# Performance work log

Measured on AMD Instinct MI355X. Metric: run time of the kernel, lower is better.

Reference implementation:

```python
import jax, jax.numpy as jnp
import numpy as np

N_NODES = 100000
N_EDGES = 1600000
N_GRAPHS = 2048
D = 128
H = 128
EPS = 1e-5


def gcn_conv(x, src, dst, W, b, n):
    # x: [N, Din], W: [Din, Dout]; GCN with added self-loops and symmetric norm
    xw = x @ W                                       # [N, Dout]
    deg = jnp.zeros((n,), x.dtype).at[dst].add(1.0) + 1.0  # deg of A+I (counted on dst)
    dinv = jax.lax.rsqrt(deg)                        # [N]
    norm = dinv[src] * dinv[dst]                     # [E]
    msg = xw[src] * norm[:, None]                    # [E, Dout] gather + scale
    agg = jax.ops.segment_sum(msg, dst, num_segments=n)
    agg = agg + xw * (dinv * dinv)[:, None]          # self-loop contribution
    return agg + b


def gru_step_h0(x, W_ih, W_hh, b_ih, b_hh):
    # single GRU step with h0 = 0 (PyTorch gate order r, z, n)
    h0 = jnp.zeros_like(x)
    gi = x @ W_ih.T + b_ih                           # [G, 3H]
    gh = h0 @ W_hh.T + b_hh                          # [G, 3H] (zeros + b_hh)
    ir, iz, inn = jnp.split(gi, 3, axis=-1)
    hr, hz, hn = jnp.split(gh, 3, axis=-1)
    r = jax.nn.sigmoid(ir + hr)
    z = jax.nn.sigmoid(iz + hz)
    n = jnp.tanh(inn + r * hn)
    return (1.0 - z) * n + z * h0


def setup_inputs() -> dict:
    key = jax.random.key(0)
    ks = jax.random.split(key, 10)
    x = jax.random.normal(ks[0], (N_NODES, D), jnp.float32)
    edge_index = jax.random.randint(ks[1], (2, N_EDGES), 0, N_NODES, jnp.int32)
    batch = jnp.sort(jax.random.randint(ks[2], (N_NODES,), 0, N_GRAPHS, jnp.int32))
    s = 1.0 / np.sqrt(H)
    return {
        "x": x,
        "edge_index": edge_index,
        "batch": batch,
        "W1": jax.random.normal(ks[3], (D, H), jnp.float32) * s,
        "b1": jnp.zeros((H,), jnp.float32),
        "W2": jax.random.normal(ks[4], (H, H), jnp.float32) * s,
        "b2": jnp.zeros((H,), jnp.float32),
        "W_ih": jax.random.normal(ks[5], (3 * H, H), jnp.float32) * s,
        "W_hh": jax.random.normal(ks[6], (3 * H, H), jnp.float32) * s,
        "b_ih": jnp.zeros((3 * H,), jnp.float32),
        "b_hh": jnp.zeros((3 * H,), jnp.float32),
        "W_lin": jax.random.normal(ks[7], (1, H), jnp.float32) * s,
        "b_lin": jnp.zeros((1,), jnp.float32),
    }


def reference(x, edge_index, batch, W1, b1, W2, b2, W_ih, W_hh, b_ih, b_hh, W_lin, b_lin):
    src, dst = edge_index[0], edge_index[1]
    n = x.shape[0]
    h = jax.nn.relu(gcn_conv(x, src, dst, W1, b1, n))
    h = gcn_conv(h, src, dst, W2, b2, n)
    # global_mean_pool over graph ids
    sums = jax.ops.segment_sum(h, batch, num_segments=N_GRAPHS)
    cnts = jax.ops.segment_sum(jnp.ones((n,), h.dtype), batch, num_segments=N_GRAPHS)
    g = sums / jnp.maximum(cnts, 1.0)[:, None]       # [G, H]
    # dropout p=0.5 in eval mode -> identity
    g = gru_step_h0(g, W_ih, W_hh, b_ih, b_hh)
    g = jax.nn.relu(g)
    mu = jnp.mean(g, axis=-1, keepdims=True)
    var = jnp.mean(jnp.square(g - mu), axis=-1, keepdims=True)
    g = (g - mu) * jax.lax.rsqrt(var + EPS)          # layer_norm, no affine
    return g @ W_lin.T + b_lin                       # [G, 1]
```

## Files before the change

### kernel.cpp

```cpp
#include <hip/hip_runtime.h>
#include <hip/hip_bf16.h>
#include <math.h>

#define DHID 128
#define SH 8
#define BIN_T 8192
#define CAPSH 13

typedef __attribute__((ext_vector_type(8))) short bf16x8;
typedef __attribute__((ext_vector_type(4))) float f32x4;

__device__ __forceinline__ int atomAddI(int* p, int v) {
    return __hip_atomic_fetch_add(p, v, __ATOMIC_RELAXED, __HIP_MEMORY_SCOPE_AGENT);
}
__device__ __forceinline__ float bf_lo(unsigned u) { return __uint_as_float(u << 16); }
__device__ __forceinline__ float bf_hi(unsigned u) { return __uint_as_float(u & 0xffff0000u); }
__device__ __forceinline__ float bf_us(unsigned short u) { return __uint_as_float((unsigned)u << 16); }
__device__ __forceinline__ unsigned short bf16_1(float f) {
    unsigned u = __float_as_uint(f);
    u += 0x7fffu + ((u >> 16) & 1u);
    return (unsigned short)(u >> 16);
}
__device__ __forceinline__ unsigned pack_bf16x2(float a, float b) {
    unsigned ua = __float_as_uint(a);
    unsigned ub = __float_as_uint(b);
    ua = (ua + 0x7fffu + ((ua >> 16) & 1u)) >> 16;
    ub = (ub + 0x7fffu + ((ub >> 16) & 1u)) & 0xffff0000u;
    return ua | ub;
}

__global__ __launch_bounds__(256) void bin_edges(const int* __restrict__ src,
                                                 const int* __restrict__ dst,
                                                 int* __restrict__ bcur,
                                                 unsigned* __restrict__ staged,
                                                 const float* __restrict__ W1,
                                                 const float* __restrict__ W2,
                                                 const float* __restrict__ Wih,
                                                 unsigned short* __restrict__ Wt1,
                                                 unsigned short* __restrict__ Wt2,
                                                 unsigned short* __restrict__ Wihb,
                                                 int E, int NB, int nb_bin) {
    int t = threadIdx.x;
    if (blockIdx.x >= nb_bin) {
        int idx = (blockIdx.x - nb_bin) * 256 + t;
        if (idx < 16384) {
            int k = idx >> 7, n = idx & 127;
            Wt1[n * 128 + k] = bf16_1(W1[idx]);
        } else if (idx < 32768) {
            int j = idx - 16384;
            int k = j >> 7, n = j & 127;
            Wt2[n * 128 + k] = bf16_1(W2[j]);
        } else if (idx < 32768 + 49152) {
            int j = idx - 32768;
            Wihb[j] = bf16_1(Wih[j]);
        }
        return;
    }
    __shared__ int lh[512], lbase[512], lcur[512];
    int e0 = blockIdx.x * BIN_T;
    int eend = min(e0 + BIN_T, E);
    for (int i = t; i < NB; i += 256) { lh[i] = 0; lcur[i] = 0; }
    __syncthreads();
    for (int e = e0 + t; e < eend; e += 256)
        atomicAdd(&lh[dst[e] >> SH], 1);
    __syncthreads();
    for (int i = t; i < NB; i += 256)
        lbase[i] = lh[i] ? atomAddI(&bcur[i], lh[i]) : 0;
    __syncthreads();
    for (int e = e0 + t; e < eend; e += 256) {
        int d = dst[e];
        int b = d >> SH;
        int pos = lbase[b] + atomicAdd(&lcur[b], 1);
        staged[((size_t)b << CAPSH) + pos] =
            (unsigned)src[e] | ((unsigned)(d & ((1 << SH) - 1)) << 24);
    }
}

__global__ __launch_bounds__(256) void scatter_csr(const unsigned* __restrict__ staged,
                                                   const int* __restrict__ bcur,
                                                   int* __restrict__ off,
                                                   float* __restrict__ dinv,
                                                   int* __restrict__ rec,
                                                   int N, int E, int NB) {
    __shared__ int sh[256];
    __shared__ int curs[256];
    __shared__ int hist[256];
    int t = threadIdx.x;
    int b = blockIdx.x;
    int node0 = b << SH;

    int s0 = (t < b) ? bcur[t] : 0;
    int s1 = (256 + t < b) ? bcur[256 + t] : 0;
    int s = s0 + s1;
#pragma unroll
    for (int o = 1; o < 64; o <<= 1) s += __shfl_xor(s, o);
    if ((t & 63) == 0) sh[t >> 6] = s;
    __syncthreads();
    int base = sh[0] + sh[1] + sh[2] + sh[3];
    __syncthreads();

    hist[t] = 0;
    __syncthreads();
    int cnt_b = bcur[b];
    const unsigned* st = staged + ((size_t)b << CAPSH);
    for (int j = t; j < cnt_b; j += 256)
        atomicAdd(&hist[st[j] >> 24], 1);
    __syncthreads();
    int v = hist[t];
    sh[t] = v;
    __syncthreads();
#pragma unroll
    for (int o = 1; o < 256; o <<= 1) {
        int x = (t >= o) ? sh[t - o] : 0;
        __syncthreads();
        sh[t] += x;
        __syncthreads();
    }
    int excl = sh[t] - v;
    int node = node0 + t;
    if (node < N) {
        off[node] = base + excl;
        dinv[node] = rsqrtf((float)v + 1.0f);
    }
    if (b == NB - 1 && t == 0) off[N] = E;
    curs[t] = base + excl;
    __syncthreads();
    for (int j = t; j < cnt_b; j += 256) {
        unsigned w = st[j];
        int dl = w >> 24;
        int pos = atomicAdd(&curs[dl], 1);
        rec[pos] = (int)(w & 0xFFFFFFu);
    }
}

__global__ __launch_bounds__(256) void gemm_mfma(const void* __restrict__ Xv,
                                                 const unsigned short* __restrict__ Wt,
                                                 unsigned short* __restrict__ Y,
                                                 int N, int x_is_bf16,
                                                 int wstride, int ystride) {
    __shared__ unsigned short Xs[64 * 136];
    __shared__ unsigned short Ws[128 * 136];
    const int tid = threadIdx.x;
    const unsigned short* Wg = Wt + (size_t)blockIdx.y * wstride;
    unsigned short* Yg = Y + (size_t)blockIdx.y * ystride;

    {
        const uint4* W4 = (const uint4*)Wg;
#pragma unroll
        for (int i = 0; i < 8; i++) {
            int idx = tid + i * 256;
            int r = idx >> 4, c8 = idx & 15;
            *(uint4*)&Ws[r * 136 + c8 * 8] = W4[idx];
        }
    }
    const int row0 = blockIdx.x * 64;
    if (x_is_bf16) {
        const uint4* X4 = (const uint4*)Xv;
#pragma unroll
        for (int i = 0; i < 4; i++) {
            int idx = tid + i * 256;
            int r = idx >> 4, c8 = idx & 15;
            uint4 v = make_uint4(0u, 0u, 0u, 0u);
            if (row0 + r < N) v = X4[(size_t)(row0 + r) * 16 + c8];
            *(uint4*)&Xs[r * 136 + c8 * 8] = v;
        }
    } else {
        const float4* X4 = (const float4*)Xv;
#pragma unroll
        for (int i = 0; i < 8; i++) {
            int idx = tid + i * 256;
            int r = idx >> 5, c4 = idx & 31;
            float4 v = make_float4(0.f, 0.f, 0.f, 0.f);
            if (row0 + r < N) v = X4[(size_t)(row0 + r) * 32 + c4];
            uint2 pk = make_uint2(pack_bf16x2(v.x, v.y), pack_bf16x2(v.z, v.w));
            *(uint2*)&Xs[r * 136 + c4 * 4] = pk;
        }
    }
    __syncthreads();

    const int lane = tid & 63;
    const int wv = tid >> 6;
    const int m = lane & 15, quad = lane >> 4;
    const int wrow = wv * 16;

    f32x4 acc[8];
#pragma unroll
    for (int i = 0; i < 8; i++) acc[i] = (f32x4){0.f, 0.f, 0.f, 0.f};

#pragma unroll
    for (int kc = 0; kc < 4; kc++) {
        bf16x8 a = *(const bf16x8*)&Xs[(wrow + m) * 136 + kc * 32 + quad * 8];
#pragma unroll
        for (int nt = 0; nt < 8; nt++) {
            bf16x8 b = *(const bf16x8*)&Ws[(nt * 16 + m) * 136 + kc * 32 + quad * 8];
            acc[nt] = __builtin_amdgcn_mfma_f32_16x16x32_bf16(a, b, acc[nt], 0, 0, 0);
        }
    }

#pragma unroll
    for (int r = 0; r < 4; r++) {
        int lrow = wrow + quad * 4 + r;
#pragma unroll
        for (int nt = 0; nt < 8; nt++)
            Xs[lrow * 136 + nt * 16 + m] = bf16_1(acc[nt][r]);
    }
    __syncthreads();
#pragma unroll
    for (int i = 0; i < 4; i++) {
        int idx = tid + i * 256;
        int r = idx >> 4, c8 = idx & 15;
        if (row0 + r < N)
            *(uint4*)&Yg[(size_t)(row0 + r) * DHID + c8 * 8] =
                *(const uint4*)&Xs[r * 136 + c8 * 8];
    }
}

__global__ __launch_bounds__(256) void aggregate(const unsigned short* __restrict__ A,
                                                 const float* __restrict__ dinv,
                                                 const int* __restrict__ off,
                                                 const int* __restrict__ rec,
                                                 const float* __restrict__ bias,
                                                 unsigned short* __restrict__ Bout,
                                                 int N, int mode) {
    int node = blockIdx.x * 4 + (threadIdx.x >> 6);
    if (node >= N) return;
    int lane = threadIdx.x & 63;
    int q  = lane >> 4;
    int ql = lane & 15;
    float di = dinv[node];
    float acc[8];
    if (q == 0) {
        float s = di * di;
        uint4 v = ((const uint4*)(A + (size_t)node * DHID))[ql];
        const float4* bb = (const float4*)(bias + ql * 8);
        float4 b0 = bb[0], b1 = bb[1];
        acc[0] = bf_lo(v.x) * s + b0.x;
        acc[1] = bf_hi(v.x) * s + b0.y;
        acc[2] = bf_lo(v.y) * s + b0.z;
        acc[3] = bf_hi(v.y) * s + b0.w;
        acc[4] = bf_lo(v.z) * s + b1.x;
        acc[5] = bf_hi(v.z) * s + b1.y;
        acc[6] = bf_lo(v.w) * s + b1.z;
        acc[7] = bf_hi(v.w) * s + b1.w;
    } else {
#pragma unroll
        for (int i = 0; i < 8; i++) acc[i] = 0.f;
    }
    int j = off[node] + q;
    int jend = off[node + 1];
    for (; j + 4 < jend; j += 8) {
        int s0 = rec[j];
        int s1 = rec[j + 4];
        uint4 v0 = ((const uint4*)(A + (size_t)s0 * DHID))[ql];
        uint4 v1 = ((const uint4*)(A + (size_t)s1 * DHID))[ql];
        float w0 = dinv[s0] * di;
        float w1 = dinv[s1] * di;
        acc[0] += bf_lo(v0.x) * w0 + bf_lo(v1.x) * w1;
        acc[1] += bf_hi(v0.x) * w0 + bf_hi(v1.x) * w1;
        acc[2] += bf_lo(v0.y) * w0 + bf_lo(v1.y) * w1;
        acc[3] += bf_hi(v0.y) * w0 + bf_hi(v1.y) * w1;
        acc[4] += bf_lo(v0.z) * w0 + bf_lo(v1.z) * w1;
        acc[5] += bf_hi(v0.z) * w0 + bf_hi(v1.z) * w1;
        acc[6] += bf_lo(v0.w) * w0 + bf_lo(v1.w) * w1;
        acc[7] += bf_hi(v0.w) * w0 + bf_hi(v1.w) * w1;
    }
    if (j < jend) {
        int s0 = rec[j];
        uint4 v0 = ((const uint4*)(A + (size_t)s0 * DHID))[ql];
        float w0 = dinv[s0] * di;
        acc[0] += bf_lo(v0.x) * w0;
        acc[1] += bf_hi(v0.x) * w0;
        acc[2] += bf_lo(v0.y) * w0;
        acc[3] += bf_hi(v0.y) * w0;
        acc[4] += bf_lo(v0.z) * w0;
        acc[5] += bf_hi(v0.z) * w0;
        acc[6] += bf_lo(v0.w) * w0;
        acc[7] += bf_hi(v0.w) * w0;
    }
#pragma unroll
    for (int i = 0; i < 8; i++) {
        acc[i] += __shfl_xor(acc[i], 16);
        acc[i] += __shfl_xor(acc[i], 32);
    }
    if (q == 0) {
        if (mode == 1) {
#pragma unroll
            for (int i = 0; i < 8; i++) acc[i] = fmaxf(acc[i], 0.f);
        }
        uint4 pk;
        pk.x = pack_bf16x2(acc[0], acc[1]);
        pk.y = pack_bf16x2(acc[2], acc[3]);
        pk.z = pack_bf16x2(acc[4], acc[5]);
        pk.w = pack_bf16x2(acc[6], acc[7]);
        ((uint4*)(Bout + (size_t)node * DHID))[ql] = pk;
    }
}

__global__ __launch_bounds__(256) void pool_mean(const unsigned short* __restrict__ B,
                                                 const int* __restrict__ batch,
                                                 float* __restrict__ g, int N, int G) {
    __shared__ int se[2];
    __shared__ float red[128];
    const int t = threadIdx.x;
    const int gr = blockIdx.x;
    if (t < 2) {
        int target = gr + t, lo = 0, hi = N;
        while (lo < hi) {
            int mid = (lo + hi) >> 1;
            if (batch[mid] < target) lo = mid + 1; else hi = mid;
        }
        se[t] = lo;
    }
    __syncthreads();
    const int s = se[0], e = se[1];
    const int col = t & 127, rh = t >> 7;
    float sum = 0.f;
    for (int r = s + rh; r < e; r += 2) sum += bf_us(B[(size_t)r * DHID + col]);
    if (rh == 1) red[col] = sum;
    __syncthreads();
    if (rh == 0) {
        float tot = sum + red[col];
        g[(size_t)gr * DHID + col] = tot / fmaxf((float)(e - s), 1.0f);
    }
}

__global__ __launch_bounds__(128) void gate_ln_head(const unsigned short* __restrict__ gi,
                                                    const float* __restrict__ b_ih,
                                                    const float* __restrict__ b_hh,
                                                    const float* __restrict__ W_lin,
                                                    const float* __restrict__ b_lin,
                                                    float* __restrict__ out, int G) {
    __shared__ float red[2];
    const int t = threadIdx.x;
    const int g = blockIdx.x;

    float d0 = bf_us(gi[(size_t)g * DHID + t]);
    float d1 = bf_us(gi[(size_t)(G + g) * DHID + t]);
    float d2 = bf_us(gi[(size_t)(2 * G + g) * DHID + t]);

    float rg = 1.f / (1.f + expf(-(d0 + b_ih[t] + b_hh[t])));
    float zg = 1.f / (1.f + expf(-(d1 + b_ih[128 + t] + b_hh[128 + t])));
    float ng = tanhf(d2 + b_ih[256 + t] + rg * b_hh[256 + t]);
    float y = fmaxf((1.f - zg) * ng, 0.f);

    auto blockSum = [&](float v) -> float {
#pragma unroll
        for (int o = 1; o < 64; o <<= 1) v += __shfl_xor(v, o);
        __syncthreads();
        if ((t & 63) == 0) red[t >> 6] = v;
        __syncthreads();
        return red[0] + red[1];
    };

    float mu = blockSum(y) * (1.f / 128.f);
    float dy = y - mu;
    float var = blockSum(dy * dy) * (1.f / 128.f);
    float yn = dy * rsqrtf(var + 1e-5f);
    float tot = blockSum(yn * W_lin[t]);
    if (t == 0) out[g] = tot + b_lin[0];
}

extern "C" void kernel_launch(void* const* d_in, const int* in_sizes, int n_in,
                              void* d_out, int out_size, void* d_ws, size_t ws_size,
                              hipStream_t stream) {
    const float* x     = (const float*)d_in[0];
    const int*   ei    = (const int*)d_in[1];
    const int*   batch = (const int*)d_in[2];
    const float* W1    = (const float*)d_in[3];
    const float* b1    = (const float*)d_in[4];
    const float* W2    = (const float*)d_in[5];
    const float* b2    = (const float*)d_in[6];
    const float* W_ih  = (const float*)d_in[7];
    const float* b_ih  = (const float*)d_in[9];
    const float* b_hh  = (const float*)d_in[10];
    const float* W_lin = (const float*)d_in[11];
    const float* b_lin = (const float*)d_in[12];
    float* out = (float*)d_out;

    const int N = in_sizes[0] / DHID;
    const int E = in_sizes[1] / 2;
    const int G = out_size;
    const int* src = ei;
    const int* dst = ei + E;
    const int NB = (N + (1 << SH) - 1) >> SH;

    auto align256 = [](size_t v) { return (v + 255) & ~(size_t)255; };
    char* p = (char*)d_ws;
    size_t used = 0;
    auto carve = [&](size_t bytes) -> char* {
        char* q = p + used;
        used += align256(bytes);
        return q;
    };

    int*   off    = (int*)carve(((size_t)N + 1) * 4);
    int*   bcur   = (int*)carve(512 * 4);
    float* dinv   = (float*)carve((size_t)N * 4);
    unsigned* staged = (unsigned*)carve(((size_t)NB << CAPSH) * 4);
    int*   rec    = (int*)carve((size_t)E * 4);
    float* gbuf   = (float*)carve((size_t)G * DHID * 4);
    unsigned short* Wt1  = (unsigned short*)carve((size_t)128 * 128 * 2);
    unsigned short* Wt2  = (unsigned short*)carve((size_t)128 * 128 * 2);
    unsigned short* Wihb = (unsigned short*)carve((size_t)3 * 128 * 128 * 2);
    unsigned short* gib  = (unsigned short*)carve((size_t)3 * G * DHID * 2);
    unsigned short* A    = (unsigned short*)carve((size_t)N * DHID * 2);
    unsigned short* B1b  = (unsigned short*)carve((size_t)N * DHID * 2);
    size_t matB = (size_t)N * DHID * 2;
    unsigned short* B2b;
    if (ws_size >= used + matB) {
        B2b = (unsigned short*)carve(matB);
    } else {
        B2b = (unsigned short*)d_in[0];
    }

    dim3 blk(256);
    int nb_g  = (N + 63) / 64;
    int nb_ag = (N + 3) / 4;
    int nb_bin = (E + BIN_T - 1) / BIN_T;
    int nb_wp  = (81920 + 255) / 256;

    hipMemsetAsync(bcur, 0, (size_t)NB * 4, stream);
    bin_edges<<<nb_bin + nb_wp, blk, 0, stream>>>(src, dst, bcur, staged,
                                                  W1, W2, W_ih, Wt1, Wt2, Wihb,
                                                  E, NB, nb_bin);
    scatter_csr<<<NB, blk, 0, stream>>>(staged, bcur, off, dinv, rec, N, E, NB);

    gemm_mfma<<<dim3(nb_g, 1), blk, 0, stream>>>(x, Wt1, A, N, 0, 0, 0);
    aggregate<<<nb_ag, blk, 0, stream>>>(A, dinv, off, rec, b1, B1b, N, 1);

    gemm_mfma<<<dim3(nb_g, 1), blk, 0, stream>>>(B1b, Wt2, A, N, 1, 0, 0);
    aggregate<<<nb_ag, blk, 0, stream>>>(A, dinv, off, rec, b2, B2b, N, 0);

    pool_mean<<<G, blk, 0, stream>>>(B2b, batch, gbuf, N, G);
    gemm_mfma<<<dim3((G + 63) / 64, 3), blk, 0, stream>>>(gbuf, Wihb, gib, G, 0,
                                                          128 * 128, G * DHID);
    gate_ln_head<<<G, dim3(128), 0, stream>>>(gib, b_ih, b_hh, W_lin, b_lin, out, G);
}
```

Measured before the change: 347.8 us.

## Simplify edge binning to per-edge global atomics and prefetch neighbor indices in aggregate

The edge-binning kernel drops its two-pass shared-memory histogram, which reserved a block-local range per bin. Each edge now takes its slot with one global atomic on the bin counter, using one thread per edge across many more blocks. Separately, the aggregation loop is software-pipelined: the next pair of neighbour indices is loaded before the current gather, and accumulators are regrouped into float2. Heavy global-atomic contention on about 391 bin counters may offset the removed passes and syncs, and the staged order inside each bin becomes nondeterministic.

```diff
diff --git a/kernel.cpp b/kernel.cpp
--- a/kernel.cpp
+++ b/kernel.cpp
@@ -4,7 +4,6 @@
 
 #define DHID 128
 #define SH 8
-#define BIN_T 8192
 #define CAPSH 13
 
 typedef __attribute__((ext_vector_type(8))) short bf16x8;
@@ -39,7 +38,7 @@
                                                  unsigned short* __restrict__ Wt1,
                                                  unsigned short* __restrict__ Wt2,
                                                  unsigned short* __restrict__ Wihb,
-                                                 int E, int NB, int nb_bin) {
+                                                 int E, int nb_bin) {
     int t = threadIdx.x;
     if (blockIdx.x >= nb_bin) {
         int idx = (blockIdx.x - nb_bin) * 256 + t;
@@ -56,24 +55,13 @@
         }
         return;
     }
-    __shared__ int lh[512], lbase[512], lcur[512];
-    int e0 = blockIdx.x * BIN_T;
-    int eend = min(e0 + BIN_T, E);
-    for (int i = t; i < NB; i += 256) { lh[i] = 0; lcur[i] = 0; }
-    __syncthreads();
-    for (int e = e0 + t; e < eend; e += 256)
-        atomicAdd(&lh[dst[e] >> SH], 1);
-    __syncthreads();
-    for (int i = t; i < NB; i += 256)
-        lbase[i] = lh[i] ? atomAddI(&bcur[i], lh[i]) : 0;
-    __syncthreads();
-    for (int e = e0 + t; e < eend; e += 256) {
-        int d = dst[e];
-        int b = d >> SH;
-        int pos = lbase[b] + atomicAdd(&lcur[b], 1);
-        staged[((size_t)b << CAPSH) + pos] =
-            (unsigned)src[e] | ((unsigned)(d & ((1 << SH) - 1)) << 24);
-    }
+    int e = blockIdx.x * 256 + t;
+    if (e >= E) return;
+    int s = src[e], d = dst[e];
+    int b = d >> SH;
+    int pos = atomAddI(&bcur[b], 1);
+    staged[((size_t)b << CAPSH) + pos] =
+        (unsigned)s | ((unsigned)(d & ((1 << SH) - 1)) << 24);
 }
 
 __global__ __launch_bounds__(256) void scatter_csr(const unsigned* __restrict__ staged,
@@ -228,70 +216,89 @@
     int q  = lane >> 4;
     int ql = lane & 15;
     float di = dinv[node];
-    float acc[8];
+    float2 acc[4];
     if (q == 0) {
         float s = di * di;
         uint4 v = ((const uint4*)(A + (size_t)node * DHID))[ql];
         const float4* bb = (const float4*)(bias + ql * 8);
         float4 b0 = bb[0], b1 = bb[1];
-        acc[0] = bf_lo(v.x) * s + b0.x;
-        acc[1] = bf_hi(v.x) * s + b0.y;
-        acc[2] = bf_lo(v.y) * s + b0.z;
-        acc[3] = bf_hi(v.y) * s + b0.w;
-        acc[4] = bf_lo(v.z) * s + b1.x;
-        acc[5] = bf_hi(v.z) * s + b1.y;
-        acc[6] = bf_lo(v.w) * s + b1.z;
-        acc[7] = bf_hi(v.w) * s + b1.w;
+        acc[0] = make_float2(bf_lo(v.x) * s + b0.x, bf_hi(v.x) * s + b0.y);
+        acc[1] = make_float2(bf_lo(v.y) * s + b0.z, bf_hi(v.y) * s + b0.w);
+        acc[2] = make_float2(bf_lo(v.z) * s + b1.x, bf_hi(v.z) * s + b1.y);
+        acc[3] = make_float2(bf_lo(v.w) * s + b1.z, bf_hi(v.w) * s + b1.w);
     } else {
 #pragma unroll
-        for (int i = 0; i < 8; i++) acc[i] = 0.f;
+        for (int i = 0; i < 4; i++) acc[i] = make_float2(0.f, 0.f);
     }
     int j = off[node] + q;
     int jend = off[node + 1];
-    for (; j + 4 < jend; j += 8) {
-        int s0 = rec[j];
-        int s1 = rec[j + 4];
-        uint4 v0 = ((const uint4*)(A + (size_t)s0 * DHID))[ql];
-        uint4 v1 = ((const uint4*)(A + (size_t)s1 * DHID))[ql];
-        float w0 = dinv[s0] * di;
-        float w1 = dinv[s1] * di;
-        acc[0] += bf_lo(v0.x) * w0 + bf_lo(v1.x) * w1;
-        acc[1] += bf_hi(v0.x) * w0 + bf_hi(v1.x) * w1;
-        acc[2] += bf_lo(v0.y) * w0 + bf_lo(v1.y) * w1;
-        acc[3] += bf_hi(v0.y) * w0 + bf_hi(v1.y) * w1;
-        acc[4] += bf_lo(v0.z) * w0 + bf_lo(v1.z) * w1;
-        acc[5] += bf_hi(v0.z) * w0 + bf_hi(v1.z) * w1;
-        acc[6] += bf_lo(v0.w) * w0 + bf_lo(v1.w) * w1;
-        acc[7] += bf_hi(v0.w) * w0 + bf_hi(v1.w) * w1;
+    if (j + 4 < jend) {
+        int s0 = rec[j], s1 = rec[j + 4];
+        for (; j + 12 < jend; j += 8) {
+            int n0 = rec[j + 8], n1 = rec[j + 12];
+            uint4 v0 = ((const uint4*)(A + (size_t)s0 * DHID))[ql];
+            uint4 v1 = ((const uint4*)(A + (size_t)s1 * DHID))[ql];
+            float w0 = dinv[s0] * di;
+            float w1 = dinv[s1] * di;
+            acc[0].x += bf_lo(v0.x) * w0 + bf_lo(v1.x) * w1;
+            acc[0].y += bf_hi(v0.x) * w0 + bf_hi(v1.x) * w1;
+            acc[1].x += bf_lo(v0.y) * w0 + bf_lo(v1.y) * w1;
+            acc[1].y += bf_hi(v0.y) * w0 + bf_hi(v1.y) * w1;
+            acc[2].x += bf_lo(v0.z) * w0 + bf_lo(v1.z) * w1;
+            acc[2].y += bf_hi(v0.z) * w0 + bf_hi(v1.z) * w1;
+            acc[3].x += bf_lo(v0.w) * w0 + bf_lo(v1.w) * w1;
+            acc[3].y += bf_hi(v0.w) * w0 + bf_hi(v1.w) * w1;
+            s0 = n0; s1 = n1;
+        }
+        {
+            uint4 v0 = ((const uint4*)(A + (size_t)s0 * DHID))[ql];
+            uint4 v1 = ((const uint4*)(A + (size_t)s1 * DHID))[ql];
+            float w0 = dinv[s0] * di;
+            float w1 = dinv[s1] * di;
+            acc[0].x += bf_lo(v0.x) * w0 + bf_lo(v1.x) * w1;
+            acc[0].y += bf_hi(v0.x) * w0 + bf_hi(v1.x) * w1;
+            acc[1].x += bf_lo(v0.y) * w0 + bf_lo(v1.y) * w1;
+            acc[1].y += bf_hi(v0.y) * w0 + bf_hi(v1.y) * w1;
+            acc[2].x += bf_lo(v0.z) * w0 + bf_lo(v1.z) * w1;
+            acc[2].y += bf_hi(v0.z) * w0 + bf_hi(v1.z) * w1;
+            acc[3].x += bf_lo(v0.w) * w0 + bf_lo(v1.w) * w1;
+            acc[3].y += bf_hi(v0.w) * w0 + bf_hi(v1.w) * w1;
+            j += 8;
+        }
     }
     if (j < jend) {
         int s0 = rec[j];
         uint4 v0 = ((const uint4*)(A + (size_t)s0 * DHID))[ql];
         float w0 = dinv[s0] * di;
-        acc[0] += bf_lo(v0.x) * w0;
-        acc[1] += bf_hi(v0.x) * w0;
-        acc[2] += bf_lo(v0.y) * w0;
-        acc[3] += bf_hi(v0.y) * w0;
-        acc[4] += bf_lo(v0.z) * w0;
-        acc[5] += bf_hi(v0.z) * w0;
-        acc[6] += bf_lo(v0.w) * w0;
-        acc[7] += bf_hi(v0.w) * w0;
-    }
-#pragma unroll
-    for (int i = 0; i < 8; i++) {
-        acc[i] += __shfl_xor(acc[i], 16);
-        acc[i] += __shfl_xor(acc[i], 32);
+        acc[0].x += bf_lo(v0.x) * w0;
+        acc[0].y += bf_hi(v0.x) * w0;
+        acc[1].x += bf_lo(v0.y) * w0;
+        acc[1].y += bf_hi(v0.y) * w0;
+        acc[2].x += bf_lo(v0.z) * w0;
+        acc[2].y += bf_hi(v0.z) * w0;
+        acc[3].x += bf_lo(v0.w) * w0;
+        acc[3].y += bf_hi(v0.w) * w0;
+    }
+#pragma unroll
+    for (int i = 0; i < 4; i++) {
+        acc[i].x += __shfl_xor(acc[i].x, 16);
+        acc[i].y += __shfl_xor(acc[i].y, 16);
+        acc[i].x += __shfl_xor(acc[i].x, 32);
+        acc[i].y += __shfl_xor(acc[i].y, 32);
     }
     if (q == 0) {
         if (mode == 1) {
 #pragma unroll
-            for (int i = 0; i < 8; i++) acc[i] = fmaxf(acc[i], 0.f);
+            for (int i = 0; i < 4; i++) {
+                acc[i].x = fmaxf(acc[i].x, 0.f);
+                acc[i].y = fmaxf(acc[i].y, 0.f);
+            }
         }
         uint4 pk;
-        pk.x = pack_bf16x2(acc[0], acc[1]);
-        pk.y = pack_bf16x2(acc[2], acc[3]);
-        pk.z = pack_bf16x2(acc[4], acc[5]);
-        pk.w = pack_bf16x2(acc[6], acc[7]);
+        pk.x = pack_bf16x2(acc[0].x, acc[0].y);
+        pk.y = pack_bf16x2(acc[1].x, acc[1].y);
+        pk.z = pack_bf16x2(acc[2].x, acc[2].y);
+        pk.w = pack_bf16x2(acc[3].x, acc[3].y);
         ((uint4*)(Bout + (size_t)node * DHID))[ql] = pk;
     }
 }
@@ -416,13 +423,13 @@
     dim3 blk(256);
     int nb_g  = (N + 63) / 64;
     int nb_ag = (N + 3) / 4;
-    int nb_bin = (E + BIN_T - 1) / BIN_T;
+    int nb_bin = (E + 255) / 256;
     int nb_wp  = (81920 + 255) / 256;
 
     hipMemsetAsync(bcur, 0, (size_t)NB * 4, stream);
     bin_edges<<<nb_bin + nb_wp, blk, 0, stream>>>(src, dst, bcur, staged,
                                                   W1, W2, W_ih, Wt1, Wt2, Wihb,
-                                                  E, NB, nb_bin);
+                                                  E, nb_bin);
     scatter_csr<<<NB, blk, 0, stream>>>(staged, bcur, off, dinv, rec, N, E, NB);
 
     gemm_mfma<<<dim3(nb_g, 1), blk, 0, stream>>>(x, Wt1, A, N, 0, 0, 0);
```

Result: slower. 866.3 us (+149.1%).
